# Kernel tuning notes

Measured on AMD Instinct MI355X. Metric: run time of the kernel, lower is better.

Reference implementation:

```python
import jax, jax.numpy as jnp
import numpy as np

VOCAB, F, H1, H2 = 64, 4096, 64, 32   # vocab size, featureVectorSize, hidden dims (hard-coded 64/32/1 in source)
NBBOX, NWORDS = 8192, 16


def _uniform(key, shape, fan_in):
    # torch nn.Linear default init: U(-1/sqrt(fan_in), 1/sqrt(fan_in))
    bound = 1.0 / np.sqrt(fan_in)
    return jax.random.uniform(key, shape, jnp.float32, -bound, bound)


def setup_inputs() -> dict:
    key = jax.random.key(0)
    ks = jax.random.split(key, 8)
    x = jax.random.normal(ks[0], (NBBOX, F), jnp.float32)
    words = jax.random.randint(ks[1], (NWORDS,), 0, VOCAB)  # indices of active word-models
    # Stacked per-word MLP params (one tiny MLP per vocab word)
    W1 = _uniform(ks[2], (VOCAB, F, H1), F)
    b1 = _uniform(ks[3], (VOCAB, H1), F)
    W2 = _uniform(ks[4], (VOCAB, H1, H2), H1)
    b2 = _uniform(ks[5], (VOCAB, H2), H1)
    W3 = _uniform(ks[6], (VOCAB, H2), H2)   # Linear(32,1) weight, squeezed to [VOCAB, H2]
    b3 = _uniform(ks[7], (VOCAB,), H2)
    return {"nBBox": NBBOX, "x": x, "words": words,
            "W1": W1, "b1": b1, "W2": W2, "b2": b2, "W3": W3, "b3": b3}


def reference(nBBox, x, words, W1, b1, W2, b2, W3, b3):
    # Gather the active word-models (dict lookup in the original)
    w1, c1 = W1[words], b1[words]          # [W,F,H1], [W,H1]
    w2, c2 = W2[words], b2[words]          # [W,H1,H2], [W,H2]
    w3, c3 = W3[words], b3[words]          # [W,H2], [W]
    # Batched 3-layer MLP over all active words at once (replaces Python loop)
    h1 = jax.nn.relu(jnp.einsum('bf,wfh->wbh', x, w1) + c1[:, None, :])   # [W,B,H1]
    h2 = jax.nn.relu(jnp.einsum('wbh,whk->wbk', h1, w2) + c2[:, None, :])  # [W,B,H2]
    logits = jnp.einsum('wbk,wk->wb', h2, w3) + c3[:, None]                # [W,B]
    # output = ones(nBBox,1) * prod_w sigmoid(logits_w)
    return jnp.prod(jax.nn.sigmoid(logits), axis=0)[:, None]               # [B,1]
```

## Files before the change

### kernel.cpp

```cpp
#include <hip/hip_runtime.h>
#include <stdint.h>
#include <math.h>

#define NBBOX 8192
#define FDIM  4096
#define H1DIM 64
#define H2DIM 32
#define NW    16

typedef __attribute__((ext_vector_type(8))) _Float16 f16x8;
typedef __attribute__((ext_vector_type(4))) float    f32x4;

typedef __attribute__((address_space(1))) void* gptr_t;
typedef __attribute__((address_space(3))) void* lptr_t;

__device__ __forceinline__ void g2l16(const void* g, void* l) {
    __builtin_amdgcn_global_load_lds((gptr_t)(uintptr_t)g,
                                     (lptr_t)(uint32_t)(uintptr_t)l,
                                     16, 0, 0);
}

__device__ __forceinline__ f16x8 cvt8(float4 a, float4 b) {
    f16x8 h;
    h[0] = (_Float16)a.x; h[1] = (_Float16)a.y; h[2] = (_Float16)a.z; h[3] = (_Float16)a.w;
    h[4] = (_Float16)b.x; h[5] = (_Float16)b.y; h[6] = (_Float16)b.z; h[7] = (_Float16)b.w;
    return h;
}

__global__ __launch_bounds__(256) void prep(
    const float* __restrict__ W1, const int* __restrict__ words,
    uint32_t* __restrict__ bth_u32)
{
    __shared__ uint32_t t[64 * 69];
    const int tid = threadIdx.x;
    const int wi = blockIdx.x >> 5;
    const int ft = blockIdx.x & 31;
    const int f0 = ft * 128;
    const int w  = words[wi];
    const int c    = tid & 63;
    const int fgrp = tid >> 6;

    const float* src = W1 + ((size_t)w * FDIM + f0) * H1DIM + c;
#pragma unroll
    for (int p = 0; p < 16; ++p) {
        const int f = fgrp * 2 + p * 8;
        float v0 = src[(size_t)f * H1DIM];
        float v1 = src[(size_t)(f + 1) * H1DIM];
        union { _Float16 h[2]; uint32_t u; } pk;
        pk.h[0] = (_Float16)v0; pk.h[1] = (_Float16)v1;
        t[c * 69 + (f >> 1)] = pk.u;
    }
    __syncthreads();
#pragma unroll
    for (int p = 0; p < 16; ++p) {
        const int cc = p * 4 + (tid >> 6);
        const int fd = tid & 63;
        bth_u32[(size_t)(wi * 64 + cc) * (FDIM / 2) + ft * 64 + fd] = t[cc * 69 + fd];
    }
}

__global__ __launch_bounds__(256, 2) void gemm_fused(
    const float* __restrict__ x, const _Float16* __restrict__ bth,
    const float* __restrict__ b1, const int* __restrict__ words,
    const float* __restrict__ W2, const float* __restrict__ b2,
    const float* __restrict__ W3, const float* __restrict__ b3,
    float* __restrict__ sig)
{
    __shared__ __align__(16) char smem[65536];
    float* tile = (float*)smem;

    const int mt   = blockIdx.x & 63;
    const int nt   = blockIdx.x >> 6;
    const int t    = threadIdx.x;
    const int w    = t >> 6;
    const int lane = t & 63;
    const int m0 = mt * 128, n0 = nt * 128;

    f32x4 acc[4][4] = {};

    const int lr = lane >> 3;
    const int cg = lane & 7;
    const float*    Ag = x   + (size_t)(m0 + w * 32 + lr) * FDIM + cg * 8;
    const _Float16* Bg = bth + (size_t)(n0 + w * 32 + lr) * FDIM + ((cg ^ lr) * 8);
    const int lwb = w * 4096;

    const int wm = w >> 1, wn = w & 1;
    const int ml = lane & 15;
    const int qw = lane >> 4;

    {
        float4 a0[8];
#pragma unroll
        for (int c = 0; c < 4; ++c) {
            a0[2 * c]     = *(const float4*)(Ag + (size_t)(c * 8) * FDIM);
            a0[2 * c + 1] = *(const float4*)(Ag + (size_t)(c * 8) * FDIM + 4);
            g2l16(Bg + (size_t)(c * 8) * FDIM, smem + 16384 + lwb + c * 1024);
        }
#pragma unroll
        for (int c = 0; c < 4; ++c)
            *(f16x8*)(smem + (w * 32 + c * 8 + lr) * 128 + ((cg ^ lr) * 16)) =
                cvt8(a0[2 * c], a0[2 * c + 1]);
    }
    __syncthreads();

    int cur = 0;
    for (int kt = 0; kt < 64; ++kt) {
        const int nb = (cur ^ 1) * 32768;
        float4 ar[8];
        if (kt < 63) {
            const size_t ko = (size_t)(kt + 1) * 64;
#pragma unroll
            for (int c = 0; c < 4; ++c) {
                ar[2 * c]     = *(const float4*)(Ag + (size_t)(c * 8) * FDIM + ko);
                ar[2 * c + 1] = *(const float4*)(Ag + (size_t)(c * 8) * FDIM + ko + 4);
                g2l16(Bg + (size_t)(c * 8) * FDIM + ko, smem + nb + 16384 + lwb + c * 1024);
            }
        }
        const _Float16* Ab = (const _Float16*)(smem + cur * 32768);
        const _Float16* Bb = (const _Float16*)(smem + cur * 32768 + 16384);
#pragma unroll
        for (int s = 0; s < 2; ++s) {
            f16x8 af[4], bfr[4];
#pragma unroll
            for (int i = 0; i < 4; ++i) {
                const int ra = wm * 64 + i * 16 + ml;
                af[i] = *(const f16x8*)&Ab[ra * 64 + (((s * 4 + qw) ^ (ml & 7)) * 8)];
            }
#pragma unroll
            for (int j = 0; j < 4; ++j) {
                const int rb = wn * 64 + j * 16 + ml;
                bfr[j] = *(const f16x8*)&Bb[rb * 64 + (((s * 4 + qw) ^ (ml & 7)) * 8)];
            }
#pragma unroll
            for (int i = 0; i < 4; ++i)
#pragma unroll
                for (int j = 0; j < 4; ++j)
                    acc[i][j] = __builtin_amdgcn_mfma_f32_16x16x32_f16(af[i], bfr[j], acc[i][j], 0, 0, 0);
        }
        if (kt < 63) {
#pragma unroll
            for (int c = 0; c < 4; ++c)
                *(f16x8*)(smem + nb + (w * 32 + c * 8 + lr) * 128 + ((cg ^ lr) * 16)) =
                    cvt8(ar[2 * c], ar[2 * c + 1]);
        }
        __syncthreads();
        cur ^= 1;
    }

    const int q  = lane >> 4;
    const int wi = nt * 2 + wn;
    const int wv = __builtin_amdgcn_readfirstlane(words[wi]);
    float* tw = tile + w * 4096;

#pragma unroll
    for (int j = 0; j < 4; ++j) {
        const int col = j * 16 + ml;
        const float bias = b1[wv * H1DIM + col];
        const int c = col >> 2, e = col & 3;
#pragma unroll
        for (int i = 0; i < 4; ++i) {
#pragma unroll
            for (int r = 0; r < 4; ++r) {
                const int row = i * 16 + q * 4 + r;
                const int pos = ((c + row) & 7) | (c & 8);
                float v = acc[i][j][r] + bias;
                tw[row * 64 + pos * 4 + e] = v > 0.f ? v : 0.f;
            }
        }
    }

    const float* W2w = W2 + (size_t)wv * (H1DIM * H2DIM);
    float a2[H2DIM];
#pragma unroll
    for (int j = 0; j < H2DIM; ++j) a2[j] = 0.f;

#pragma unroll
    for (int c2 = 0; c2 < 16; ++c2) {
        const int pos = ((c2 + lane) & 7) | (c2 & 8);
        f32x4 h = *(const f32x4*)&tw[lane * 64 + pos * 4];
#pragma unroll
        for (int kk = 0; kk < 4; ++kk) {
            const float hv = h[kk];
            const int k = c2 * 4 + kk;
#pragma unroll
            for (int j = 0; j < H2DIM; ++j)
                a2[j] = fmaf(hv, W2w[k * H2DIM + j], a2[j]);
        }
    }

    float logit = b3[wv];
#pragma unroll
    for (int j = 0; j < H2DIM; ++j) {
        float h2 = a2[j] + b2[wv * H2DIM + j];
        h2 = h2 > 0.f ? h2 : 0.f;
        logit = fmaf(h2, W3[wv * H2DIM + j], logit);
    }
    sig[(size_t)wi * NBBOX + m0 + wm * 64 + lane] = 1.f / (1.f + expf(-logit));
}

__global__ void prod_k(const float* __restrict__ sig, float* __restrict__ out) {
    const int r = blockIdx.x * 256 + threadIdx.x;
    float p = 1.f;
#pragma unroll
    for (int wi = 0; wi < NW; ++wi) p *= sig[(size_t)wi * NBBOX + r];
    out[r] = p;
}

extern "C" void kernel_launch(void* const* d_in, const int* in_sizes, int n_in,
                              void* d_out, int out_size, void* d_ws, size_t ws_size,
                              hipStream_t stream)
{
    const float* x   = (const float*)d_in[1];
    const int* words = (const int*)  d_in[2];
    const float* W1  = (const float*)d_in[3];
    const float* b1  = (const float*)d_in[4];
    const float* W2  = (const float*)d_in[5];
    const float* b2  = (const float*)d_in[6];
    const float* W3  = (const float*)d_in[7];
    const float* b3  = (const float*)d_in[8];
    float* out = (float*)d_out;

    char* ws = (char*)d_ws;
    _Float16* bth = (_Float16*)(ws);
    float*    sig = (float*)   (ws + 8388608);

    prep<<<512, 256, 0, stream>>>(W1, words, (uint32_t*)bth);
    gemm_fused<<<512, 256, 0, stream>>>(x, bth, b1, words, W2, b2, W3, b3, sig);
    prod_k<<<NBBOX / 256, 256, 0, stream>>>(sig, out);
}
```

Baseline: 347.5 us.

## Prefetch A tiles two stages ahead in registers with unrolled double-buffer loop

The GEMM main loop is unrolled by two and uses two register sets for the fp32 A tiles, so global loads of A are issued two K-steps ahead instead of one. Each converted tile is written to LDS before the MFMA phase rather than after it. Scheduling barriers stop the compiler from mixing the staging code into the MFMA block. The aim is to hide global-load latency behind a full iteration of compute, at the cost of roughly 64 extra VGPRs per thread.

Result: no change. 349.9 us (+0.7%).

```diff
diff --git a/kernel.cpp b/kernel.cpp
--- a/kernel.cpp
+++ b/kernel.cpp
@@ -88,64 +88,85 @@
     const int ml = lane & 15;
     const int qw = lane >> 4;
 
-    {
-        float4 a0[8];
-#pragma unroll
-        for (int c = 0; c < 4; ++c) {
-            a0[2 * c]     = *(const float4*)(Ag + (size_t)(c * 8) * FDIM);
-            a0[2 * c + 1] = *(const float4*)(Ag + (size_t)(c * 8) * FDIM + 4);
-            g2l16(Bg + (size_t)(c * 8) * FDIM, smem + 16384 + lwb + c * 1024);
-        }
-#pragma unroll
-        for (int c = 0; c < 4; ++c)
-            *(f16x8*)(smem + (w * 32 + c * 8 + lr) * 128 + ((cg ^ lr) * 16)) =
-                cvt8(a0[2 * c], a0[2 * c + 1]);
-    }
-    __syncthreads();
-
-    int cur = 0;
-    for (int kt = 0; kt < 64; ++kt) {
-        const int nb = (cur ^ 1) * 32768;
-        float4 ar[8];
-        if (kt < 63) {
-            const size_t ko = (size_t)(kt + 1) * 64;
-#pragma unroll
-            for (int c = 0; c < 4; ++c) {
-                ar[2 * c]     = *(const float4*)(Ag + (size_t)(c * 8) * FDIM + ko);
-                ar[2 * c + 1] = *(const float4*)(Ag + (size_t)(c * 8) * FDIM + ko + 4);
-                g2l16(Bg + (size_t)(c * 8) * FDIM + ko, smem + nb + 16384 + lwb + c * 1024);
-            }
-        }
-        const _Float16* Ab = (const _Float16*)(smem + cur * 32768);
-        const _Float16* Bb = (const _Float16*)(smem + cur * 32768 + 16384);
-#pragma unroll
-        for (int s = 0; s < 2; ++s) {
-            f16x8 af[4], bfr[4];
-#pragma unroll
-            for (int i = 0; i < 4; ++i) {
-                const int ra = wm * 64 + i * 16 + ml;
-                af[i] = *(const f16x8*)&Ab[ra * 64 + (((s * 4 + qw) ^ (ml & 7)) * 8)];
-            }
-#pragma unroll
-            for (int j = 0; j < 4; ++j) {
-                const int rb = wn * 64 + j * 16 + ml;
-                bfr[j] = *(const f16x8*)&Bb[rb * 64 + (((s * 4 + qw) ^ (ml & 7)) * 8)];
-            }
-#pragma unroll
-            for (int i = 0; i < 4; ++i)
-#pragma unroll
-                for (int j = 0; j < 4; ++j)
-                    acc[i][j] = __builtin_amdgcn_mfma_f32_16x16x32_f16(af[i], bfr[j], acc[i][j], 0, 0, 0);
-        }
-        if (kt < 63) {
-#pragma unroll
-            for (int c = 0; c < 4; ++c)
-                *(f16x8*)(smem + nb + (w * 32 + c * 8 + lr) * 128 + ((cg ^ lr) * 16)) =
-                    cvt8(ar[2 * c], ar[2 * c + 1]);
-        }
+    float4 rA[8], rB[8];
+
+#define STAGE_A_LOAD(R, KT) do { \
+    _Pragma("unroll") \
+    for (int c = 0; c < 4; ++c) { \
+        const float* ap = Ag + (size_t)(c * 8) * FDIM + (size_t)(KT) * 64; \
+        R[2 * c]     = *(const float4*)(ap); \
+        R[2 * c + 1] = *(const float4*)(ap + 4); \
+    } } while (0)
+
+#define STAGE_B(KT, NB) do { \
+    _Pragma("unroll") \
+    for (int c = 0; c < 4; ++c) \
+        g2l16(Bg + (size_t)(c * 8) * FDIM + (size_t)(KT) * 64, \
+              smem + (NB) + 16384 + lwb + c * 1024); \
+    } while (0)
+
+#define WRITE_A(R, NB) do { \
+    _Pragma("unroll") \
+    for (int c = 0; c < 4; ++c) \
+        *(f16x8*)(smem + (NB) + (w * 32 + c * 8 + lr) * 128 + ((cg ^ lr) * 16)) = \
+            cvt8(R[2 * c], R[2 * c + 1]); \
+    } while (0)
+
+#define MFMA_PHASE(BUF) do { \
+    const _Float16* Ab = (const _Float16*)(smem + (BUF)); \
+    const _Float16* Bb = (const _Float16*)(smem + (BUF) + 16384); \
+    _Pragma("unroll") \
+    for (int s = 0; s < 2; ++s) { \
+        f16x8 af[4], bfr[4]; \
+        _Pragma("unroll") \
+        for (int i = 0; i < 4; ++i) { \
+            const int ra = wm * 64 + i * 16 + ml; \
+            af[i] = *(const f16x8*)&Ab[ra * 64 + (((s * 4 + qw) ^ (ml & 7)) * 8)]; \
+        } \
+        _Pragma("unroll") \
+        for (int j = 0; j < 4; ++j) { \
+            const int rb = wn * 64 + j * 16 + ml; \
+            bfr[j] = *(const f16x8*)&Bb[rb * 64 + (((s * 4 + qw) ^ (ml & 7)) * 8)]; \
+        } \
+        _Pragma("unroll") \
+        for (int i = 0; i < 4; ++i) \
+            _Pragma("unroll") \
+            for (int j = 0; j < 4; ++j) \
+                acc[i][j] = __builtin_amdgcn_mfma_f32_16x16x32_f16(af[i], bfr[j], acc[i][j], 0, 0, 0); \
+    } } while (0)
+
+    STAGE_A_LOAD(rA, 0);
+    STAGE_B(0, 0);
+    WRITE_A(rA, 0);
+    STAGE_A_LOAD(rB, 1);
+    __syncthreads();
+
+    for (int kt = 0; kt < 62; kt += 2) {
+        STAGE_A_LOAD(rA, kt + 2);
+        STAGE_B(kt + 1, 32768);
+        WRITE_A(rB, 32768);
+        __builtin_amdgcn_sched_barrier(0);
+        MFMA_PHASE(0);
         __syncthreads();
-        cur ^= 1;
-    }
+        STAGE_A_LOAD(rB, kt + 3);
+        STAGE_B(kt + 2, 0);
+        WRITE_A(rA, 0);
+        __builtin_amdgcn_sched_barrier(0);
+        MFMA_PHASE(32768);
+        __syncthreads();
+    }
+    STAGE_B(63, 32768);
+    WRITE_A(rB, 32768);
+    __builtin_amdgcn_sched_barrier(0);
+    MFMA_PHASE(0);
+    __syncthreads();
+    MFMA_PHASE(32768);
+    __syncthreads();
+
+#undef STAGE_A_LOAD
+#undef STAGE_B
+#undef WRITE_A
+#undef MFMA_PHASE
 
     const int q  = lane >> 4;
     const int wi = nt * 2 + wn;
```
